# Kernel tuning notes

Measured on AMD Instinct MI355X. Metric: run time of the kernel, lower is better.

## Reference

```python
import jax, jax.numpy as jnp
import numpy as np

T, B, I, H = 512, 64, 1024, 1024


def setup_inputs() -> dict:
    key = jax.random.key(0)
    ks = jax.random.split(key, 9)
    g_x = 1.0 / np.sqrt(I)   # glorot-ish scale
    g_h = 1.0 / np.sqrt(H)
    return {
        "X": jax.random.normal(ks[0], (T, B, I), dtype=jnp.float32),
        "Wa_x": jax.random.normal(ks[1], (I, H), dtype=jnp.float32) * g_x,
        "Wi_x": jax.random.normal(ks[2], (I, H), dtype=jnp.float32) * g_x,
        "Wf_x": jax.random.normal(ks[3], (I, H), dtype=jnp.float32) * g_x,
        "Wo_x": jax.random.normal(ks[4], (I, H), dtype=jnp.float32) * g_x,
        "Wa_h": jax.random.normal(ks[5], (H, H), dtype=jnp.float32) * g_h,
        "Wi_h": jax.random.normal(ks[6], (H, H), dtype=jnp.float32) * g_h,
        "Wf_h": jax.random.normal(ks[7], (H, H), dtype=jnp.float32) * g_h,
        "Wo_h": jax.random.normal(ks[8], (H, H), dtype=jnp.float32) * g_h,
        "ba": jnp.zeros((H,), dtype=jnp.float32),
        "bi": jnp.zeros((H,), dtype=jnp.float32),
        "bf": jnp.zeros((H,), dtype=jnp.float32),
        "bo": jnp.zeros((H,), dtype=jnp.float32),
    }


def reference(X, Wa_x, Wi_x, Wf_x, Wo_x, Wa_h, Wi_h, Wf_h, Wo_h, ba, bi, bf, bo):
    # Fuse the 4 input-to-gate GEMMs across all timesteps (no recurrence there):
    # Xg: [T, B, 4H] with gate order (a, i, f, o)
    Wx = jnp.concatenate([Wa_x, Wi_x, Wf_x, Wo_x], axis=1)  # [I, 4H]
    Wh = jnp.concatenate([Wa_h, Wi_h, Wf_h, Wo_h], axis=1)  # [H, 4H]
    b = jnp.concatenate([ba, bi, bf, bo], axis=0)           # [4H]
    Xg = jnp.einsum("tbi,ig->tbg", X, Wx) + b               # [T, B, 4H]

    Hd = Wa_h.shape[0]

    def step(carry, xg):
        h, s = carry
        g = xg + h @ Wh  # [B, 4H]; at t=0, h=0 so matches the t==0 branch
        a = jnp.tanh(g[:, 0 * Hd:1 * Hd])
        i = jax.nn.sigmoid(g[:, 1 * Hd:2 * Hd])
        f = jax.nn.sigmoid(g[:, 2 * Hd:3 * Hd])
        o = jax.nn.sigmoid(g[:, 3 * Hd:4 * Hd])
        s_new = a * i + s * f
        h_new = jnp.tanh(s_new) * o
        return (h_new, s_new), h_new

    Bsz = X.shape[1]
    init = (jnp.zeros((Bsz, Hd), X.dtype), jnp.zeros((Bsz, Hd), X.dtype))
    _, outputs = jax.lax.scan(step, init, Xg)  # [T, B, H]
    return outputs


if __name__ == "__main__":
    out = reference(**setup_inputs())
    print(out.shape)
```

## Files before the change

kernel.cpp:

```cpp
#include <hip/hip_runtime.h>
#include <hip/hip_bf16.h>

typedef __bf16 bf8 __attribute__((ext_vector_type(8)));
typedef float  f32x4 __attribute__((ext_vector_type(4)));
typedef unsigned long long u64;

#define TT 512
#define BBATCH 64
#define IDIM 1024
#define HDIM 1024
#define G4 4096
#define NREC 128

__device__ __forceinline__ float sigf(float x) {
  x = fminf(fmaxf(x, -30.f), 30.f);
  return 1.f / (1.f + __expf(-x));
}
__device__ __forceinline__ float tanh_(float x) {
  x = fminf(fmaxf(x, -15.f), 15.f);
  float e = __expf(2.f * x);
  return (e - 1.f) / (e + 1.f);
}
__device__ __forceinline__ f32x4 MFMA(bf8 a, bf8 b, f32x4 c) {
  return __builtin_amdgcn_mfma_f32_16x16x32_bf16(a, b, c, 0, 0, 0);
}

__global__ __launch_bounds__(256) void k_convw(
    const float* __restrict__ s0, const float* __restrict__ s1,
    const float* __restrict__ s2, const float* __restrict__ s3,
    const float* __restrict__ s4, const float* __restrict__ s5,
    const float* __restrict__ s6, const float* __restrict__ s7,
    __bf16* __restrict__ WxT, __bf16* __restrict__ WhT) {
  int z = blockIdx.z;
  const float* src = (z == 0) ? s0 : (z == 1) ? s1 : (z == 2) ? s2 :
                     (z == 3) ? s3 : (z == 4) ? s4 : (z == 5) ? s5 :
                     (z == 6) ? s6 : s7;
  __bf16* dst = (z < 4) ? WxT : WhT;
  int j0 = blockIdx.x * 64, k0 = blockIdx.y * 64;
  __shared__ float T[64][65];
  int tid = threadIdx.x;
#pragma unroll
  for (int i = 0; i < 16; ++i) {
    int idx = tid + i * 256;
    int kl = idx >> 6, jl = idx & 63;
    T[kl][jl] = src[(size_t)(k0 + kl) * 1024 + j0 + jl];
  }
  __syncthreads();
#pragma unroll
  for (int i = 0; i < 2; ++i) {
    int Gt = tid + i * 256;
    int nl = Gt >> 3, gq = Gt & 7;
    int n = (z & 3) * 1024 + j0 + nl;
    bf8 v;
#pragma unroll
    for (int e = 0; e < 8; ++e) v[e] = (__bf16)T[gq * 8 + e][nl];
    *(bf8*)&dst[(size_t)n * 1024 + k0 + gq * 8] = v;
  }
}

__global__ void k_bias(const float* __restrict__ b0, const float* __restrict__ b1,
                       const float* __restrict__ b2, const float* __restrict__ b3,
                       float* __restrict__ bias) {
  int i = blockIdx.x * 256 + threadIdx.x;
  if (i < G4) {
    const float* s = (i < 1024) ? b0 : (i < 2048) ? b1 : (i < 3072) ? b2 : b3;
    bias[i] = s[i & 1023];
  }
}

__global__ __launch_bounds__(512, 1) void k_fused(
    const float* __restrict__ Xg_r, float* __restrict__ Xg_w,
    const __bf16* __restrict__ WhT, const __bf16* __restrict__ WxT,
    const float* __restrict__ Xnext, const float* __restrict__ bias,
    __bf16* __restrict__ hb0, __bf16* __restrict__ hb1,
    float* __restrict__ S, float* __restrict__ out,
    int* flags, int t0, int Tc, int nrec, int gM) {
  __shared__ char smem[65536];
  const int bid = blockIdx.x, tid = threadIdx.x;
  const int lane = tid & 63, w = tid >> 6;

  if (bid < nrec) {
    bf8 (*Ls)[128] = (bf8(*)[128])smem;
    float* Gsf = (float*)smem;
    const int kh = w >> 1, bh = w & 1;
    const int rh = bid & 1, hc0 = (bid >> 1) * 16;
    const int l15 = lane & 15, lq = lane >> 4;
    const int rowbase = rh * 32;
    const int br = bh * 16 + l15;

    bf8 Bf[32];
#pragma unroll
    for (int ct = 0; ct < 4; ++ct)
#pragma unroll
      for (int s = 0; s < 8; ++s)
        Bf[ct * 8 + s] = *(const bf8*)&WhT[(size_t)(ct * 1024 + hc0 + l15) * 1024 +
                                           kh * 256 + s * 32 + lq * 8];
#pragma unroll
    for (int i = 0; i < 32; ++i) {
      float4 t = __builtin_bit_cast(float4, Bf[i]);
      asm volatile("" : "+v"(t.x), "+v"(t.y), "+v"(t.z), "+v"(t.w));
      Bf[i] = __builtin_bit_cast(bf8, t);
    }

    const int er = tid >> 4, ec = tid & 15;
    float sreg = 0.f;
    if (t0 > 0) sreg = S[(size_t)(rowbase + er) * 1024 + hc0 + ec];

    for (int lt = 0; lt < Tc; ++lt) {
      const int t = t0 + lt;

      const float* xp = Xg_r + ((size_t)lt * 64 + rowbase + er) * G4 + hc0 + ec;
      float xa = xp[0], xi = xp[1024], xf = xp[2048], xo = xp[3072];

      if (t > 0) {
        if (lt > 0) {
          int v0, v1;
          do {
            v0 = __hip_atomic_load(flags + lane * 32, __ATOMIC_RELAXED,
                                   __HIP_MEMORY_SCOPE_AGENT);
            v1 = __hip_atomic_load(flags + (lane + 64) * 32, __ATOMIC_RELAXED,
                                   __HIP_MEMORY_SCOPE_AGENT);
          } while (!__all(v0 >= t && v1 >= t));
          asm volatile("" ::: "memory");
        }
        const __bf16* hp = ((t - 1) & 1) ? hb1 : hb0;

        union { u64 q[2]; bf8 v; } vv[8];
#pragma unroll
        for (int i = 0; i < 8; ++i) {
          int g = i * 512 + tid;
          const u64* sp = (const u64*)(hp + (size_t)(rowbase + (g >> 7)) * 1024 +
                                       (g & 127) * 8);
          vv[i].q[0] = __hip_atomic_load((u64*)sp, __ATOMIC_RELAXED,
                                         __HIP_MEMORY_SCOPE_AGENT);
          vv[i].q[1] = __hip_atomic_load((u64*)sp + 1, __ATOMIC_RELAXED,
                                         __HIP_MEMORY_SCOPE_AGENT);
        }
#pragma unroll
        for (int i = 0; i < 8; ++i) {
          int g = i * 512 + tid, r = g >> 7, cg = g & 127;
          Ls[r][cg ^ (r & 7)] = vv[i].v;
        }
        __syncthreads();

        f32x4 a0 = {}, a1 = {}, a2 = {}, a3 = {};
#pragma unroll
        for (int s = 0; s < 8; ++s) {
          bf8 af = Ls[br][(kh * 32 + s * 4 + lq) ^ (br & 7)];
          a0 = MFMA(af, Bf[s], a0);
          a1 = MFMA(af, Bf[8 + s], a1);
          a2 = MFMA(af, Bf[16 + s], a2);
          a3 = MFMA(af, Bf[24 + s], a3);
        }
        __syncthreads();

        {
          float* G = Gsf + kh * (32 * 68) + (bh * 16 + lq * 4) * 68 + l15;
#pragma unroll
          for (int q = 0; q < 4; ++q) {
            G[q * 68 + 0]  = a0[q];
            G[q * 68 + 16] = a1[q];
            G[q * 68 + 32] = a2[q];
            G[q * 68 + 48] = a3[q];
          }
        }
        __syncthreads();

        const float* Gr = Gsf + er * 68 + ec;
#pragma unroll
        for (int k2 = 0; k2 < 4; ++k2) {
          xa += Gr[k2 * 2176 + 0];
          xi += Gr[k2 * 2176 + 16];
          xf += Gr[k2 * 2176 + 32];
          xo += Gr[k2 * 2176 + 48];
        }
      }

      float av = tanh_(xa), iv = sigf(xi), fv = sigf(xf), ov = sigf(xo);
      sreg = av * iv + sreg * fv;
      float h0 = tanh_(sreg) * ov;

      out[((size_t)t * 64 + rowbase + er) * 1024 + hc0 + ec] = h0;

      float hnb = __shfl(h0, lane + 1);
      if ((ec & 1) == 0) {
        unsigned int pv =
            (unsigned int)__builtin_bit_cast(unsigned short, (__bf16)h0) |
            ((unsigned int)__builtin_bit_cast(unsigned short, (__bf16)hnb) << 16);
        __bf16* hn = (t & 1) ? hb1 : hb0;
        __hip_atomic_store(
            (unsigned int*)((char*)hn + ((size_t)(rowbase + er) * 1024 + hc0 + ec) * 2),
            pv, __ATOMIC_RELAXED, __HIP_MEMORY_SCOPE_AGENT);
      }

      __syncthreads();
      if (tid == 0)
        __hip_atomic_store(flags + bid * 32, t + 1, __ATOMIC_RELAXED,
                           __HIP_MEMORY_SCOPE_AGENT);
    }

    S[(size_t)(rowbase + er) * 1024 + hc0 + ec] = sreg;
    return;
  }

  if (gM == 0) return;
  const int nw = gridDim.x - nrec;
  const int wid = bid - nrec;
  __bf16 (*As)[40] = (__bf16(*)[40])smem;
  __bf16 (*Bs)[40] = (__bf16(*)[40])(smem + 128 * 40 * 2);
  const int wr = (w >> 2) * 64, wc = (w & 3) * 32;
  const int sm = tid >> 2, sk = (tid & 3) * 8;
  const int gl15 = lane & 15, glq = lane >> 4;
  const int ntiles = (gM / 128) * (G4 / 128);

  for (int tile = wid; tile < ntiles; tile += nw) {
    const int m0 = (tile >> 5) * 128, n0 = (tile & 31) * 128;
    const float*  Ap = Xnext + (size_t)(m0 + sm) * 1024 + sk;
    const __bf16* Bp = WxT + (size_t)(n0 + sm) * 1024 + sk;
    f32x4 acc[4][2] = {};
    float4 ra0, ra1;
    bf8 rb;
    auto ld = [&](int kt) {
      ra0 = *(const float4*)(Ap + kt * 32);
      ra1 = *(const float4*)(Ap + kt * 32 + 4);
      rb = *(const bf8*)(Bp + kt * 32);
    };
    ld(0);
    for (int kt = 0; kt < 32; ++kt) {
      __syncthreads();
      bf8 va;
      va[0]=(__bf16)ra0.x; va[1]=(__bf16)ra0.y; va[2]=(__bf16)ra0.z; va[3]=(__bf16)ra0.w;
      va[4]=(__bf16)ra1.x; va[5]=(__bf16)ra1.y; va[6]=(__bf16)ra1.z; va[7]=(__bf16)ra1.w;
      *(bf8*)&As[sm][sk] = va;
      *(bf8*)&Bs[sm][sk] = rb;
      if (kt < 31) ld(kt + 1);
      __syncthreads();
      bf8 af[4], bv[2];
#pragma unroll
      for (int r = 0; r < 4; ++r) af[r] = *(const bf8*)&As[wr + r * 16 + gl15][glq * 8];
#pragma unroll
      for (int c = 0; c < 2; ++c) bv[c] = *(const bf8*)&Bs[wc + c * 16 + gl15][glq * 8];
#pragma unroll
      for (int r = 0; r < 4; ++r)
#pragma unroll
        for (int c = 0; c < 2; ++c)
          acc[r][c] = MFMA(af[r], bv[c], acc[r][c]);
    }
#pragma unroll
    for (int c = 0; c < 2; ++c) {
      int col = n0 + wc + c * 16 + gl15;
      float bc = bias[col];
#pragma unroll
      for (int r = 0; r < 4; ++r)
#pragma unroll
        for (int q = 0; q < 4; ++q)
          Xg_w[(size_t)(m0 + wr + r * 16 + glq * 4 + q) * G4 + col] = acc[r][c][q] + bc;
    }
    __syncthreads();
  }
}

extern "C" void kernel_launch(void* const* d_in, const int* in_sizes, int n_in,
                              void* d_out, int out_size, void* d_ws, size_t ws_size,
                              hipStream_t stream) {
  const float* X  = (const float*)d_in[0];
  const float* wa = (const float*)d_in[1];
  const float* wi = (const float*)d_in[2];
  const float* wf = (const float*)d_in[3];
  const float* wo = (const float*)d_in[4];
  const float* ha = (const float*)d_in[5];
  const float* hi = (const float*)d_in[6];
  const float* hf = (const float*)d_in[7];
  const float* ho = (const float*)d_in[8];
  const float* b0 = (const float*)d_in[9];
  const float* b1 = (const float*)d_in[10];
  const float* b2 = (const float*)d_in[11];
  const float* b3 = (const float*)d_in[12];
  float* out = (float*)d_out;
  char* ws = (char*)d_ws;

  size_t off = 0;
  auto alloc = [&](size_t bytes) {
    void* p = ws + off;
    off += (bytes + 255) & ~(size_t)255;
    return p;
  };
  __bf16* WxT = (__bf16*)alloc((size_t)G4 * IDIM * 2);
  __bf16* WhT = (__bf16*)alloc((size_t)G4 * HDIM * 2);
  float* bias = (float*)alloc(G4 * 4);
  float* S    = (float*)alloc((size_t)BBATCH * HDIM * 4);
  __bf16* hb0 = (__bf16*)alloc((size_t)BBATCH * HDIM * 2);
  __bf16* hb1 = (__bf16*)alloc((size_t)BBATCH * HDIM * 2);
  int* flags  = (int*)alloc(NREC * 32 * 4);
  size_t base = off;

  const size_t perXg = (size_t)BBATCH * G4 * 4;
  int Tc = 64;
  while (Tc > 4 && base + 2 * (size_t)Tc * perXg > ws_size) Tc >>= 1;
  float* Xg0 = (float*)(ws + base);
  float* Xg1 = (float*)(ws + base + (size_t)Tc * perXg);
  int nchunks = TT / Tc;

  k_convw<<<dim3(16, 16, 8), dim3(256), 0, stream>>>(wa, wi, wf, wo, ha, hi, hf,
                                                     ho, WxT, WhT);
  k_bias<<<dim3(16), dim3(256), 0, stream>>>(b0, b1, b2, b3, bias);
  hipMemsetAsync(flags, 0, NREC * 32 * 4, stream);

  k_fused<<<dim3(256), dim3(512), 0, stream>>>(
      nullptr, Xg0, WhT, WxT, X, bias, hb0, hb1, S, out, flags,
      0, 0, 0, Tc * BBATCH);

  for (int c = 0; c < nchunks; ++c) {
    float* xr = (c & 1) ? Xg1 : Xg0;
    float* xw = (c & 1) ? Xg0 : Xg1;
    int gM = (c + 1 < nchunks) ? Tc * BBATCH : 0;
    const float* Xn = X + (size_t)(c + 1) * Tc * BBATCH * IDIM;
    k_fused<<<dim3(256), dim3(512), 0, stream>>>(
        xr, xw, WhT, WxT, Xn, bias, hb0, hb1, S, out, flags,
        c * Tc, Tc, NREC, gM);
  }
}
```

Measured before the change: 2.364 ms.

## Repartition recurrent MFMA work by gate and K-half, wait only on same-row-half flags

Each wave now owns one gate column tile and half of K, computing both 16-row batch halves. This halves the register-resident weight fragments per lane and cuts the cross-wave K reduction from four partials to two. The flag spin now polls only the 64 producer blocks that share this block's row half instead of all 128. Launch bounds are raised to allow two blocks per CU, which changes register allocation and may affect co-residency of the persistent recurrent blocks.

```diff
diff --git a/kernel.cpp b/kernel.cpp
--- a/kernel.cpp
+++ b/kernel.cpp
@@ -68,7 +68,7 @@
   }
 }
 
-__global__ __launch_bounds__(512, 1) void k_fused(
+__global__ __launch_bounds__(512, 2) void k_fused(
     const float* __restrict__ Xg_r, float* __restrict__ Xg_w,
     const __bf16* __restrict__ WhT, const __bf16* __restrict__ WxT,
     const float* __restrict__ Xnext, const float* __restrict__ bias,
@@ -82,24 +82,21 @@
   if (bid < nrec) {
     bf8 (*Ls)[128] = (bf8(*)[128])smem;
     float* Gsf = (float*)smem;
-    const int kh = w >> 1, bh = w & 1;
+    const int ct = w & 3, kh = w >> 2;
     const int rh = bid & 1, hc0 = (bid >> 1) * 16;
     const int l15 = lane & 15, lq = lane >> 4;
     const int rowbase = rh * 32;
-    const int br = bh * 16 + l15;
-
-    bf8 Bf[32];
-#pragma unroll
-    for (int ct = 0; ct < 4; ++ct)
-#pragma unroll
-      for (int s = 0; s < 8; ++s)
-        Bf[ct * 8 + s] = *(const bf8*)&WhT[(size_t)(ct * 1024 + hc0 + l15) * 1024 +
-                                           kh * 256 + s * 32 + lq * 8];
-#pragma unroll
-    for (int i = 0; i < 32; ++i) {
-      float4 t = __builtin_bit_cast(float4, Bf[i]);
-      asm volatile("" : "+v"(t.x), "+v"(t.y), "+v"(t.z), "+v"(t.w));
-      Bf[i] = __builtin_bit_cast(bf8, t);
+
+    bf8 Bf[16];
+#pragma unroll
+    for (int s = 0; s < 16; ++s)
+      Bf[s] = *(const bf8*)&WhT[(size_t)(ct * 1024 + hc0 + l15) * 1024 +
+                                kh * 512 + s * 32 + lq * 8];
+#pragma unroll
+    for (int i = 0; i < 16; ++i) {
+      float4 tpin = __builtin_bit_cast(float4, Bf[i]);
+      asm volatile("" : "+v"(tpin.x), "+v"(tpin.y), "+v"(tpin.z), "+v"(tpin.w));
+      Bf[i] = __builtin_bit_cast(bf8, tpin);
     }
 
     const int er = tid >> 4, ec = tid & 15;
@@ -112,15 +109,15 @@
       const float* xp = Xg_r + ((size_t)lt * 64 + rowbase + er) * G4 + hc0 + ec;
       float xa = xp[0], xi = xp[1024], xf = xp[2048], xo = xp[3072];
 
+      f32x4 acc0 = {}, acc1 = {};
+
       if (t > 0) {
         if (lt > 0) {
-          int v0, v1;
+          int v;
           do {
-            v0 = __hip_atomic_load(flags + lane * 32, __ATOMIC_RELAXED,
-                                   __HIP_MEMORY_SCOPE_AGENT);
-            v1 = __hip_atomic_load(flags + (lane + 64) * 32, __ATOMIC_RELAXED,
-                                   __HIP_MEMORY_SCOPE_AGENT);
-          } while (!__all(v0 >= t && v1 >= t));
+            v = __hip_atomic_load(flags + (2 * lane + rh) * 32, __ATOMIC_RELAXED,
+                                  __HIP_MEMORY_SCOPE_AGENT);
+          } while (!__all(v >= t));
           asm volatile("" ::: "memory");
         }
         const __bf16* hp = ((t - 1) & 1) ? hb1 : hb0;
@@ -143,37 +140,31 @@
         }
         __syncthreads();
 
-        f32x4 a0 = {}, a1 = {}, a2 = {}, a3 = {};
-#pragma unroll
-        for (int s = 0; s < 8; ++s) {
-          bf8 af = Ls[br][(kh * 32 + s * 4 + lq) ^ (br & 7)];
-          a0 = MFMA(af, Bf[s], a0);
-          a1 = MFMA(af, Bf[8 + s], a1);
-          a2 = MFMA(af, Bf[16 + s], a2);
-          a3 = MFMA(af, Bf[24 + s], a3);
+#pragma unroll
+        for (int s = 0; s < 16; ++s) {
+          int kk = kh * 64 + s * 4 + lq;
+          bf8 af0 = Ls[l15][kk ^ (l15 & 7)];
+          bf8 af1 = Ls[16 + l15][kk ^ (l15 & 7)];
+          acc0 = MFMA(af0, Bf[s], acc0);
+          acc1 = MFMA(af1, Bf[s], acc1);
         }
         __syncthreads();
 
         {
-          float* G = Gsf + kh * (32 * 68) + (bh * 16 + lq * 4) * 68 + l15;
+          float* G = Gsf + kh * 2176 + ct * 16 + l15;
 #pragma unroll
           for (int q = 0; q < 4; ++q) {
-            G[q * 68 + 0]  = a0[q];
-            G[q * 68 + 16] = a1[q];
-            G[q * 68 + 32] = a2[q];
-            G[q * 68 + 48] = a3[q];
+            G[(lq * 4 + q) * 68]        = acc0[q];
+            G[(16 + lq * 4 + q) * 68]   = acc1[q];
           }
         }
         __syncthreads();
 
         const float* Gr = Gsf + er * 68 + ec;
-#pragma unroll
-        for (int k2 = 0; k2 < 4; ++k2) {
-          xa += Gr[k2 * 2176 + 0];
-          xi += Gr[k2 * 2176 + 16];
-          xf += Gr[k2 * 2176 + 32];
-          xo += Gr[k2 * 2176 + 48];
-        }
+        xa += Gr[0]  + Gr[2176 + 0];
+        xi += Gr[16] + Gr[2176 + 16];
+        xf += Gr[32] + Gr[2176 + 32];
+        xo += Gr[48] + Gr[2176 + 48];
       }
 
       float av = tanh_(xa), iv = sigf(xi), fv = sigf(xf), ov = sigf(xo);
```

Measured after the change: 2.227 ms. -5.8%, faster.
